# Kernel tuning notes

Measured on AMD Instinct MI355X. Metric: run time of the kernel, lower is better.

The kernel has to match this reference:

```python
import jax, jax.numpy as jnp
import numpy as np

# pywt db4 decomposition filters (dec_lo, dec_hi), 8 taps
DEC_LO = np.array([-0.010597401784997278, 0.032883011666982945, 0.030841381835986965,
                   -0.18703481171888114, -0.02798376941698385, 0.6308807679295904,
                   0.7148465705525415, 0.23037781330885523])
DEC_HI = np.array([-0.23037781330885523, 0.7148465705525415, -0.6308807679295904,
                   -0.02798376941698385, 0.18703481171888114, 0.030841381835986965,
                   -0.032883011666982945, -0.010597401784997278])
HEADS = 8


def dwt_db4(v):
    # Equivalent of pywt.dwt(v, 'db4') (mode='symmetric') applied along last axis.
    # Symmetric (half-point) extension by L-1=7, full convolution, downsample taking
    # every 2nd sample starting at conv index 1 -> out_len = floor((n+7)/2).
    pad = [(0, 0)] * (v.ndim - 1) + [(7, 7)]
    ext = jnp.pad(v, pad, mode='symmetric')[..., 1:]
    lead = v.shape[:-1]
    lhs = ext.reshape(-1, 1, ext.shape[-1])                       # (N, 1, n+13)
    rhs = jnp.stack([jnp.asarray(DEC_LO[::-1], v.dtype),
                     jnp.asarray(DEC_HI[::-1], v.dtype)])[:, None, :]  # (2, 1, 8)
    out = jax.lax.conv_general_dilated(lhs, rhs, (2,), 'VALID')   # (N, 2, out_len)
    out = out.reshape(*lead, 2, -1)
    return out[..., 0, :], out[..., 1, :]


def setup_inputs() -> dict:
    key = jax.random.key(0)
    k0, k1, k2, k3 = jax.random.split(key, 4)
    B, S, H = 4, 2048, 1024
    a = float(np.sqrt(6.0 / (H + H)))  # xavier_uniform bound
    x = jax.random.normal(k0, (B, S, H), dtype=jnp.float32)
    Wq = jax.random.uniform(k1, (H, H), jnp.float32, -a, a)
    Wk = jax.random.uniform(k2, (H, H), jnp.float32, -a, a)
    Wv = jax.random.uniform(k3, (H, H), jnp.float32, -a, a)
    return {"x": x, "Wq": Wq, "Wk": Wk, "Wv": Wv}


def reference(x, Wq, Wk, Wv):
    B, S, Hd = x.shape
    H = HEADS
    dk = Hd // H
    scale = dk ** -0.5
    # torch nn.Linear: y = x @ W.T
    q = (x @ Wq.T).reshape(B, S, H, dk).transpose(0, 2, 1, 3) * scale  # (B,H,S,dk)
    k = (x @ Wk.T).reshape(B, S, H, dk).transpose(0, 2, 1, 3)
    v = (x @ Wv.T).reshape(B, S, H, dk).transpose(0, 2, 1, 3)
    attn = jax.nn.softmax(jnp.einsum('bhqd,bhkd->bhqk', q, k), axis=-1)
    cA, cD = dwt_db4(v)                                   # (B,H,S,wA) each
    wA = cA.shape[-1]
    wcD = jnp.einsum('bhqk,bhkw->bhqw', attn, cD)
    out1 = wcD.transpose(0, 2, 1, 3).reshape(B, S, H * wA)
    out2 = cA.reshape(-1, S, H * wA)                      # faithful raw view of (B,H,S,wA)
    return out1, out2
```

## Files before the change

kernel.cpp:

```cpp
#include <hip/hip_runtime.h>
#include <hip/hip_bf16.h>

#define B_ 4
#define S_ 2048
#define HD 1024
#define NH 8
#define DK 128
#define WA 67
#define WPAD 80

typedef __attribute__((ext_vector_type(8))) short short8;
typedef __attribute__((ext_vector_type(4))) short short4v;
typedef __attribute__((ext_vector_type(4))) float floatx4;

__device__ __forceinline__ float hexp2(float x) { return __builtin_amdgcn_exp2f(x); }

__device__ __forceinline__ short f2bf(float f) {
    union { float f; unsigned u; } c; c.f = f;
    unsigned u = c.u;
    u += 0x7FFF + ((u >> 16) & 1);
    return (short)(u >> 16);
}
__device__ __forceinline__ float bf2f(short s) {
    union { unsigned u; float f; } c; c.u = ((unsigned)(unsigned short)s) << 16;
    return c.f;
}
__device__ __forceinline__ short f2bf_trunc(float f) {
    union { float f; unsigned u; } c; c.f = f;
    return (short)(c.u >> 16);
}

__device__ __forceinline__ void glds16(void* lds, const void* g) {
    __builtin_amdgcn_global_load_lds(
        (const __attribute__((address_space(1))) unsigned*)g,
        (__attribute__((address_space(3))) unsigned*)lds, 16, 0, 0);
}

__device__ __constant__ float FLO[8] = {
    0.23037781330885523f,  0.7148465705525415f,  0.6308807679295904f,
   -0.02798376941698385f, -0.18703481171888114f, 0.030841381835986965f,
    0.032883011666982945f, -0.010597401784997278f };
__device__ __constant__ float FHI[8] = {
   -0.010597401784997278f, -0.032883011666982945f, 0.030841381835986965f,
    0.18703481171888114f,  -0.02798376941698385f, -0.6308807679295904f,
    0.7148465705525415f,   -0.23037781330885523f };

__global__ __launch_bounds__(256) void cvt_all(
    const float* __restrict__ x,  const float* __restrict__ wq,
    const float* __restrict__ wk, const float* __restrict__ wv,
    short* __restrict__ xb, short* __restrict__ wb)
{
    const size_t w_elems = (size_t)HD * HD;
    int blk = blockIdx.x;
    const float* src; short* dst; int lb;
    if (blk < 4096)      { src = x;  dst = xb;               lb = blk; }
    else if (blk < 4608) { src = wq; dst = wb;               lb = blk - 4096; }
    else if (blk < 5120) { src = wk; dst = wb + w_elems;     lb = blk - 4608; }
    else                 { src = wv; dst = wb + 2 * w_elems; lb = blk - 5120; }
    int i = lb * 256 + threadIdx.x;
    const float4* s = (const float4*)src + (size_t)i * 2;
    float4 f0 = s[0], f1 = s[1];
    short8 o;
    o[0] = f2bf(f0.x); o[1] = f2bf(f0.y); o[2] = f2bf(f0.z); o[3] = f2bf(f0.w);
    o[4] = f2bf(f1.x); o[5] = f2bf(f1.y); o[6] = f2bf(f1.z); o[7] = f2bf(f1.w);
    *((short8*)dst + i) = o;
}

__global__ __launch_bounds__(256) void qkv_gemm(
    const short* __restrict__ xb, const short* __restrict__ Wb,
    short* __restrict__ Qb, short* __restrict__ Kb,
    float* __restrict__ outA, short* __restrict__ cdt)
{
    __shared__ __align__(16) short smem[128 * 134];
    short* As = smem;
    short* Bs = smem + 128 * 64;
    short* Cs = smem;
    const int tid  = threadIdx.x;
    const int wv   = tid >> 6;
    const int lane = tid & 63;
    const int l15  = lane & 15;
    const int quad = lane >> 4;
    const int m0 = blockIdx.x * 128;
    const int n0 = blockIdx.y * 128;
    const int z  = blockIdx.z;
    const short* W = Wb + (size_t)z * HD * HD;
    const float scale = (z == 0) ? 0.12751743786072596f : 1.0f;
    const int wm = (wv & 1) * 64;
    const int wn = (wv >> 1) * 64;
    const int srow = lane >> 3;
    const int sch  = (lane & 7) ^ (srow & 7);
    const int rxor = (l15 & 7);

    floatx4 acc[4][4] = {};
    for (int kk = 0; kk < HD; kk += 64) {
        __syncthreads();
        #pragma unroll
        for (int i = 0; i < 4; ++i) {
            int ti = wv * 4 + i;
            int r  = ti * 8 + srow;
            glds16(As + ti * 512, xb + (size_t)(m0 + r) * HD + kk + sch * 8);
            glds16(Bs + ti * 512, W  + (size_t)(n0 + r) * HD + kk + sch * 8);
        }
        __syncthreads();
        #pragma unroll
        for (int s4 = 0; s4 < 2; ++s4) {
            short8 a[4], b[4];
            #pragma unroll
            for (int t = 0; t < 4; ++t) {
                int ch = (s4 * 4 + quad) ^ rxor;
                a[t] = *(const short8*)&As[(wm + t * 16 + l15) * 64 + ch * 8];
                b[t] = *(const short8*)&Bs[(wn + t * 16 + l15) * 64 + ch * 8];
            }
            #pragma unroll
            for (int mt = 0; mt < 4; ++mt)
                #pragma unroll
                for (int nt = 0; nt < 4; ++nt)
                    acc[mt][nt] = __builtin_amdgcn_mfma_f32_16x16x32_bf16(
                        a[mt], b[nt], acc[mt][nt], 0, 0, 0);
        }
    }
    if (z != 2) {
        short* Yb = (z == 0) ? Qb : Kb;
        #pragma unroll
        for (int mt = 0; mt < 4; ++mt)
            #pragma unroll
            for (int nt = 0; nt < 4; ++nt)
                #pragma unroll
                for (int reg = 0; reg < 4; ++reg) {
                    int rg = m0 + wm + mt * 16 + quad * 4 + reg;
                    int cg = n0 + wn + nt * 16 + l15;
                    int b = rg >> 11, s = rg & 2047;
                    int h = cg >> 7,  d = cg & 127;
                    Yb[((size_t)(b * NH + h) * S_ + s) * DK + d] =
                        f2bf(acc[mt][nt][reg] * scale);
                }
        return;
    }
    __syncthreads();
    #pragma unroll
    for (int mt = 0; mt < 4; ++mt)
        #pragma unroll
        for (int nt = 0; nt < 4; ++nt)
            #pragma unroll
            for (int reg = 0; reg < 4; ++reg)
                Cs[(wm + mt * 16 + quad * 4 + reg) * 134 + wn + nt * 16 + l15] =
                    f2bf(acc[mt][nt][reg]);
    __syncthreads();
    const int rl    = tid & 127;
    const int chunk = tid >> 7;
    const int rg = m0 + rl;
    const int b = rg >> 11, s = rg & 2047;
    const int bh = b * NH + blockIdx.y;
    const short* vr = Cs + rl * 134;
    auto getv = [&](int i) -> float {
        int k = (i < 6) ? (5 - i) : (i < 134) ? (i - 6) : (261 - i);
        return bf2f(vr[k]);
    };
    const int t0 = chunk * 34;
    const int t1 = (chunk == 0) ? 34 : WA;
    float win[8];
    #pragma unroll
    for (int j = 0; j < 8; ++j) win[j] = getv(2 * t0 + j);
    float* oA = outA + ((size_t)bh * S_ + s) * WA;
    for (int t = t0; t < t1; ++t) {
        float lo = 0.f, hi = 0.f;
        #pragma unroll
        for (int j = 0; j < 8; ++j) { lo += win[j] * FLO[j]; hi += win[j] * FHI[j]; }
        oA[t] = lo;
        cdt[((size_t)bh * WPAD + t) * S_ + s] = f2bf(hi);
        #pragma unroll
        for (int j = 0; j < 6; ++j) win[j] = win[j + 2];
        if (t + 1 < t1) { win[6] = getv(2 * t + 8); win[7] = getv(2 * t + 9); }
    }
    if (chunk == 1) {
        #pragma unroll
        for (int w = WA; w < WPAD; ++w)
            cdt[((size_t)bh * WPAD + w) * S_ + s] =
                (w == 67) ? (short)0x3F80 : (short)0;
    }
}

__global__ __launch_bounds__(256, 2) void attn_kernel(
    const short* __restrict__ Qb, const short* __restrict__ Kb,
    const short* __restrict__ cdt, float* __restrict__ out1)
{
    __shared__ __align__(16) short Ks[64 * 128];
    __shared__ __align__(16) short Ds[WPAD * 64];
    __shared__ __align__(16) short Pt[8 * 1024];
    const int tid  = threadIdx.x;
    const int wv   = tid >> 6;
    const int lane = tid & 63;
    const int l15  = lane & 15;
    const int quad = lane >> 4;
    const int qt = blockIdx.x;
    const int bh = blockIdx.y;
    const int b = bh >> 3, h = bh & 7;
    const int rxor = l15 & 7;

    short8 aq[2][4];
    #pragma unroll
    for (int n = 0; n < 2; ++n) {
        const short* qrow =
            Qb + ((size_t)bh * S_ + qt * 128 + wv * 32 + n * 16 + l15) * DK;
        #pragma unroll
        for (int s4 = 0; s4 < 4; ++s4)
            aq[n][s4] = *(const short8*)(qrow + s4 * 32 + quad * 8);
    }

    floatx4 O[2][5] = {};

    const short* kbase = Kb + (size_t)bh * S_ * DK;
    const int krow = lane >> 4;
    const int kch  = (lane & 15);
    const int drow = lane >> 3;
    const int dch  = (lane & 7) ^ (drow & 7);
    short* ptw = Pt + wv * 2048;

    for (int kt = 0; kt < 32; ++kt) {
        __syncthreads();
        #pragma unroll
        for (int i = 0; i < 4; ++i) {
            int ti = wv * 4 + i;
            int r  = ti * 4 + krow;
            int ch = kch ^ (r & 7);
            glds16(Ks + ti * 512, kbase + ((size_t)kt * 64 + r) * DK + ch * 8);
        }
        #pragma unroll
        for (int i = 0; i < 3; ++i) {
            int t = wv + i * 4;
            if (t < 10) {
                int r = t * 8 + drow;
                glds16(Ds + t * 512,
                       cdt + ((size_t)bh * WPAD + r) * S_ + kt * 64 + dch * 8);
            }
        }
        __syncthreads();

        floatx4 sc[2][4] = {};
        #pragma unroll
        for (int s4 = 0; s4 < 4; ++s4) {
            short8 kf[4];
            #pragma unroll
            for (int mt = 0; mt < 4; ++mt) {
                int ch = (s4 * 4 + quad) ^ rxor;
                kf[mt] = *(const short8*)&Ks[(mt * 16 + l15) * 128 + ch * 8];
            }
            #pragma unroll
            for (int n = 0; n < 2; ++n)
                #pragma unroll
                for (int mt = 0; mt < 4; ++mt)
                    sc[n][mt] = __builtin_amdgcn_mfma_f32_16x16x32_bf16(
                        kf[mt], aq[n][s4], sc[n][mt], 0, 0, 0);
        }
        #pragma unroll
        for (int n = 0; n < 2; ++n) {
            #pragma unroll
            for (int mt = 0; mt < 4; ++mt) {
                short4v pk;
                #pragma unroll
                for (int reg = 0; reg < 4; ++reg)
                    pk[reg] = f2bf_trunc(hexp2(sc[n][mt][reg]));
                int ch = (mt * 2 + (quad >> 1)) ^ rxor;
                *(short4v*)&ptw[n * 1024 + l15 * 64 + ch * 8 + (quad & 1) * 4] = pk;
            }
        }
        short8 ap[2][2];
        #pragma unroll
        for (int mt = 0; mt < 2; ++mt)
            #pragma unroll
            for (int ks = 0; ks < 2; ++ks) {
                int ch = (ks * 4 + quad) ^ rxor;
                ap[mt][ks] = *(const short8*)&ptw[mt * 1024 + l15 * 64 + ch * 8];
            }
        #pragma unroll
        for (int j = 0; j < 5; ++j) {
            #pragma unroll
            for (int ks = 0; ks < 2; ++ks) {
                int ch = (ks * 4 + quad) ^ rxor;
                short8 bd = *(const short8*)&Ds[(j * 16 + l15) * 64 + ch * 8];
                #pragma unroll
                for (int mt = 0; mt < 2; ++mt)
                    O[mt][j] = __builtin_amdgcn_mfma_f32_16x16x32_bf16(
                        ap[mt][ks], bd, O[mt][j], 0, 0, 0);
            }
        }
    }
    float rl[2][4];
    #pragma unroll
    for (int mt = 0; mt < 2; ++mt)
        #pragma unroll
        for (int reg = 0; reg < 4; ++reg)
            rl[mt][reg] = 1.0f / __shfl(O[mt][4][reg], (quad << 4) | 3, 64);
    #pragma unroll
    for (int mt = 0; mt < 2; ++mt)
        #pragma unroll
        for (int j = 0; j < 5; ++j) {
            int w = j * 16 + l15;
            if (w < WA) {
                #pragma unroll
                for (int reg = 0; reg < 4; ++reg) {
                    int qrow_g = qt * 128 + wv * 32 + mt * 16 + quad * 4 + reg;
                    out1[((size_t)(b * S_ + qrow_g)) * (NH * WA) + h * WA + w] =
                        O[mt][j][reg] * rl[mt][reg];
                }
            }
        }
}

extern "C" void kernel_launch(void* const* d_in, const int* in_sizes, int n_in,
                              void* d_out, int out_size, void* d_ws, size_t ws_size,
                              hipStream_t stream)
{
    const float* x  = (const float*)d_in[0];
    const float* Wq = (const float*)d_in[1];
    const float* Wk = (const float*)d_in[2];
    const float* Wv = (const float*)d_in[3];
    float* out = (float*)d_out;

    const size_t x_elems   = (size_t)B_ * S_ * HD;
    const size_t w_elems   = (size_t)HD * HD;
    const size_t qkv_elems = (size_t)B_ * NH * S_ * DK;
    short* xb  = (short*)d_ws;
    short* Wb  = xb + x_elems;
    short* Qb  = Wb + 3 * w_elems;
    short* Kb  = Qb + qkv_elems;
    short* cdt = Kb + qkv_elems;
    float* out1 = out;
    float* out2 = out + (size_t)B_ * S_ * NH * WA;

    cvt_all<<<dim3(5632), 256, 0, stream>>>(x, Wq, Wk, Wv, xb, Wb);
    qkv_gemm<<<dim3(64, 8, 3), 256, 0, stream>>>(xb, Wb, Qb, Kb, out2, cdt);
    attn_kernel<<<dim3(16, 32), 256, 0, stream>>>(Qb, Kb, cdt, out1);
}
```

Before: 229.7 us.

## Fold db4 DWT filters into V weights and merge into one GEMM

Because the wavelet transform is linear along the head dimension, the low-pass and high-pass filters (with symmetric extension) are folded into Wv in the prep kernel. This produces two 536-row filtered weight matrices, so cA and cD come straight out of an extended GEMM (26 column tiles in one launch). It removes the per-row serial DWT epilogue, the LDS staging of V and the extra syncs in the V blocks. The cost is extra GEMM work from padded 640-row weight tiles and less coalesced strided cD stores. The cD padding rows are now filled by the prep kernel.

After: 246.9 us. 7.5% more time.

```diff
diff --git a/kernel.cpp b/kernel.cpp
--- a/kernel.cpp
+++ b/kernel.cpp
@@ -8,6 +8,7 @@
 #define DK 128
 #define WA 67
 #define WPAD 80
+#define NWROWS 640
 
 typedef __attribute__((ext_vector_type(8))) short short8;
 typedef __attribute__((ext_vector_type(4))) short short4v;
@@ -45,45 +46,83 @@
     0.18703481171888114f,  -0.02798376941698385f, -0.6308807679295904f,
     0.7148465705525415f,   -0.23037781330885523f };
 
-__global__ __launch_bounds__(256) void cvt_all(
+__global__ __launch_bounds__(256) void prep_all(
     const float* __restrict__ x,  const float* __restrict__ wq,
     const float* __restrict__ wk, const float* __restrict__ wv,
-    short* __restrict__ xb, short* __restrict__ wb)
+    short* __restrict__ xb, short* __restrict__ wqk,
+    short* __restrict__ wa, short* __restrict__ wg, short* __restrict__ cdt)
 {
     const size_t w_elems = (size_t)HD * HD;
     int blk = blockIdx.x;
-    const float* src; short* dst; int lb;
-    if (blk < 4096)      { src = x;  dst = xb;               lb = blk; }
-    else if (blk < 4608) { src = wq; dst = wb;               lb = blk - 4096; }
-    else if (blk < 5120) { src = wk; dst = wb + w_elems;     lb = blk - 4608; }
-    else                 { src = wv; dst = wb + 2 * w_elems; lb = blk - 5120; }
-    int i = lb * 256 + threadIdx.x;
-    const float4* s = (const float4*)src + (size_t)i * 2;
-    float4 f0 = s[0], f1 = s[1];
-    short8 o;
-    o[0] = f2bf(f0.x); o[1] = f2bf(f0.y); o[2] = f2bf(f0.z); o[3] = f2bf(f0.w);
-    o[4] = f2bf(f1.x); o[5] = f2bf(f1.y); o[6] = f2bf(f1.z); o[7] = f2bf(f1.w);
-    *((short8*)dst + i) = o;
-}
-
-__global__ __launch_bounds__(256) void qkv_gemm(
-    const short* __restrict__ xb, const short* __restrict__ Wb,
+    if (blk < 5120) {
+        const float* src; short* dst; int lb;
+        if (blk < 4096)      { src = x;  dst = xb;            lb = blk; }
+        else if (blk < 4608) { src = wq; dst = wqk;           lb = blk - 4096; }
+        else                 { src = wk; dst = wqk + w_elems; lb = blk - 4608; }
+        int i = lb * 256 + threadIdx.x;
+        const float4* s = (const float4*)src + (size_t)i * 2;
+        float4 f0 = s[0], f1 = s[1];
+        short8 o;
+        o[0] = f2bf(f0.x); o[1] = f2bf(f0.y); o[2] = f2bf(f0.z); o[3] = f2bf(f0.w);
+        o[4] = f2bf(f1.x); o[5] = f2bf(f1.y); o[6] = f2bf(f1.z); o[7] = f2bf(f1.w);
+        *((short8*)dst + i) = o;
+    } else if (blk < 5388) {
+        int idx = (blk - 5120) * 256 + threadIdx.x;
+        int j  = idx >> 7;
+        int c0 = (idx & 127) * 8;
+        unsigned h = (unsigned)j / 67u;
+        unsigned t = (unsigned)j - h * 67u;
+        float aa[8] = {}, gg[8] = {};
+        #pragma unroll
+        for (int jj = 0; jj < 8; ++jj) {
+            int i = 2 * (int)t + jj;
+            int k = (i < 6) ? (5 - i) : (i < 134) ? (i - 6) : (261 - i);
+            const float4* wr =
+                (const float4*)(wv + ((size_t)(h * 128 + k)) * HD + c0);
+            float4 v0 = wr[0], v1 = wr[1];
+            float fl = FLO[jj], fh = FHI[jj];
+            aa[0] += fl * v0.x; aa[1] += fl * v0.y; aa[2] += fl * v0.z; aa[3] += fl * v0.w;
+            aa[4] += fl * v1.x; aa[5] += fl * v1.y; aa[6] += fl * v1.z; aa[7] += fl * v1.w;
+            gg[0] += fh * v0.x; gg[1] += fh * v0.y; gg[2] += fh * v0.z; gg[3] += fh * v0.w;
+            gg[4] += fh * v1.x; gg[5] += fh * v1.y; gg[6] += fh * v1.z; gg[7] += fh * v1.w;
+        }
+        short8 oa, og;
+        #pragma unroll
+        for (int q = 0; q < 8; ++q) { oa[q] = f2bf(aa[q]); og[q] = f2bf(gg[q]); }
+        *(short8*)&wa[(size_t)j * HD + c0] = oa;
+        *(short8*)&wg[(size_t)j * HD + c0] = og;
+    } else {
+        int idx = (blk - 5388) * 256 + threadIdx.x;
+        int within = idx * 8;
+        int row = within >> 11;
+        int s0  = within & 2047;
+        int bh = row / 13, tr = row - bh * 13;
+        short val = (tr == 0) ? (short)0x3F80 : (short)0;
+        short8 o = { val, val, val, val, val, val, val, val };
+        *(short8*)&cdt[((size_t)bh * WPAD + 67 + tr) * S_ + s0] = o;
+    }
+}
+
+__global__ __launch_bounds__(256) void mega_gemm(
+    const short* __restrict__ xb, const short* __restrict__ wqk,
+    const short* __restrict__ wa, const short* __restrict__ wg,
     short* __restrict__ Qb, short* __restrict__ Kb,
-    float* __restrict__ outA, short* __restrict__ cdt)
+    float* __restrict__ out2, short* __restrict__ cdt)
 {
-    __shared__ __align__(16) short smem[128 * 134];
-    short* As = smem;
-    short* Bs = smem + 128 * 64;
-    short* Cs = smem;
+    __shared__ __align__(16) short As[128 * 64];
+    __shared__ __align__(16) short Bs[128 * 64];
     const int tid  = threadIdx.x;
     const int wv   = tid >> 6;
     const int lane = tid & 63;
     const int l15  = lane & 15;
     const int quad = lane >> 4;
     const int m0 = blockIdx.x * 128;
-    const int n0 = blockIdx.y * 128;
-    const int z  = blockIdx.z;
-    const short* W = Wb + (size_t)z * HD * HD;
+    const int y  = blockIdx.y;
+    int z, n0; const short* W;
+    if (y < 8)       { z = 0; n0 = y * 128;        W = wqk; }
+    else if (y < 16) { z = 1; n0 = (y - 8) * 128;  W = wqk + (size_t)HD * HD; }
+    else if (y < 21) { z = 2; n0 = (y - 16) * 128; W = wa; }
+    else             { z = 3; n0 = (y - 21) * 128; W = wg; }
     const float scale = (z == 0) ? 0.12751743786072596f : 1.0f;
     const int wm = (wv & 1) * 64;
     const int wn = (wv >> 1) * 64;
@@ -119,7 +158,7 @@
                         a[mt], b[nt], acc[mt][nt], 0, 0, 0);
         }
     }
-    if (z != 2) {
+    if (z < 2) {
         short* Yb = (z == 0) ? Qb : Kb;
         #pragma unroll
         for (int mt = 0; mt < 4; ++mt)
@@ -134,49 +173,27 @@
                     Yb[((size_t)(b * NH + h) * S_ + s) * DK + d] =
                         f2bf(acc[mt][nt][reg] * scale);
                 }
-        return;
-    }
-    __syncthreads();
-    #pragma unroll
-    for (int mt = 0; mt < 4; ++mt)
-        #pragma unroll
-        for (int nt = 0; nt < 4; ++nt)
-            #pragma unroll
-            for (int reg = 0; reg < 4; ++reg)
-                Cs[(wm + mt * 16 + quad * 4 + reg) * 134 + wn + nt * 16 + l15] =
-                    f2bf(acc[mt][nt][reg]);
-    __syncthreads();
-    const int rl    = tid & 127;
-    const int chunk = tid >> 7;
-    const int rg = m0 + rl;
-    const int b = rg >> 11, s = rg & 2047;
-    const int bh = b * NH + blockIdx.y;
-    const short* vr = Cs + rl * 134;
-    auto getv = [&](int i) -> float {
-        int k = (i < 6) ? (5 - i) : (i < 134) ? (i - 6) : (261 - i);
-        return bf2f(vr[k]);
-    };
-    const int t0 = chunk * 34;
-    const int t1 = (chunk == 0) ? 34 : WA;
-    float win[8];
-    #pragma unroll
-    for (int j = 0; j < 8; ++j) win[j] = getv(2 * t0 + j);
-    float* oA = outA + ((size_t)bh * S_ + s) * WA;
-    for (int t = t0; t < t1; ++t) {
-        float lo = 0.f, hi = 0.f;
-        #pragma unroll
-        for (int j = 0; j < 8; ++j) { lo += win[j] * FLO[j]; hi += win[j] * FHI[j]; }
-        oA[t] = lo;
-        cdt[((size_t)bh * WPAD + t) * S_ + s] = f2bf(hi);
-        #pragma unroll
-        for (int j = 0; j < 6; ++j) win[j] = win[j + 2];
-        if (t + 1 < t1) { win[6] = getv(2 * t + 8); win[7] = getv(2 * t + 9); }
-    }
-    if (chunk == 1) {
-        #pragma unroll
-        for (int w = WA; w < WPAD; ++w)
-            cdt[((size_t)bh * WPAD + w) * S_ + s] =
-                (w == 67) ? (short)0x3F80 : (short)0;
+    } else {
+        #pragma unroll
+        for (int mt = 0; mt < 4; ++mt)
+            #pragma unroll
+            for (int nt = 0; nt < 4; ++nt)
+                #pragma unroll
+                for (int reg = 0; reg < 4; ++reg) {
+                    int rg = m0 + wm + mt * 16 + quad * 4 + reg;
+                    int j  = n0 + wn + nt * 16 + l15;
+                    if (j < NH * WA) {
+                        int b = rg >> 11, s = rg & 2047;
+                        unsigned h = (unsigned)j / 67u;
+                        unsigned t = (unsigned)j - h * 67u;
+                        if (z == 2)
+                            out2[((size_t)(b * NH + (int)h) * S_ + s) * WA + t] =
+                                acc[mt][nt][reg];
+                        else
+                            cdt[((size_t)(b * NH + (int)h) * WPAD + t) * S_ + s] =
+                                f2bf(acc[mt][nt][reg]);
+                    }
+                }
     }
 }
 
@@ -321,14 +338,16 @@
     const size_t w_elems   = (size_t)HD * HD;
     const size_t qkv_elems = (size_t)B_ * NH * S_ * DK;
     short* xb  = (short*)d_ws;
-    short* Wb  = xb + x_elems;
-    short* Qb  = Wb + 3 * w_elems;
+    short* Wqk = xb + x_elems;
+    short* Wa  = Wqk + 2 * w_elems;
+    short* Wg  = Wa + (size_t)NWROWS * HD;
+    short* Qb  = Wg + (size_t)NWROWS * HD;
     short* Kb  = Qb + qkv_elems;
     short* cdt = Kb + qkv_elems;
     float* out1 = out;
     float* out2 = out + (size_t)B_ * S_ * NH * WA;
 
-    cvt_all<<<dim3(5632), 256, 0, stream>>>(x, Wq, Wk, Wv, xb, Wb);
-    qkv_gemm<<<dim3(64, 8, 3), 256, 0, stream>>>(xb, Wb, Qb, Kb, out2, cdt);
+    prep_all<<<dim3(5804), 256, 0, stream>>>(x, Wq, Wk, Wv, xb, Wqk, Wa, Wg, cdt);
+    mega_gemm<<<dim3(64, 26), 256, 0, stream>>>(xb, Wqk, Wa, Wg, Qb, Kb, out2, cdt);
     attn_kernel<<<dim3(16, 32), 256, 0, stream>>>(Qb, Kb, cdt, out1);
 }
```
